# Performance work log

Hardware: AMD Instinct MI355X
Metric: run time of the kernel (lower is better)

The kernel has to match this reference:

```python
import jax, jax.numpy as jnp
import numpy as np

N = 8192          # num_points
RADIUS = 0.5


def _make_curve(num_points):
    # Reproduces the interp1d-based turbo-coil curve from __init__ (linear interp).
    xk = np.array([-2, -1, 0, 1, 1, 0, -1, -1, 0, 1, 2], dtype=np.float64)
    zk = np.array([0, 0, 1, 0, -1, 0, 1, 0, -1, 0, 0], dtype=np.float64)
    yk = np.array([0, 0, 1, 1, -1, -1, -1, 1, 1, 0, 0], dtype=np.float64)
    t = np.linspace(0.0, 1.0, len(xk))
    s = np.linspace(0.0, 1.0, num_points)
    return (np.interp(s, t, xk).astype(np.float32),
            np.interp(s, t, yk).astype(np.float32),
            np.interp(s, t, zk).astype(np.float32))


def setup_inputs() -> dict:
    x, y, z = _make_curve(N)
    return {"x": jnp.asarray(x), "y": jnp.asarray(y), "z": jnp.asarray(z)}


def _cdist(a, b):
    # pairwise Euclidean distance, safe at zero (subgradient 0 like torch.cdist)
    d2 = jnp.sum(a * a, -1, keepdims=True) - 2.0 * (a @ b.T) + jnp.sum(b * b, -1)
    d2 = jnp.maximum(d2, 0.0)
    safe = jnp.where(d2 > 0.0, d2, 1.0)
    return jnp.where(d2 > 0.0, jnp.sqrt(safe), 0.0)


def _mask_distances(dist, min_dist):
    # Original: for each row i, scan j = i, i+1, ... and overwrite entries with
    # min_dist+1 while dist[i,j] <= min_dist, breaking at the first entry that
    # exceeds min_dist (the j in range(i,0) loop is empty, so only the forward
    # scan matters). Vectorized: contiguous prefix-run starting at the diagonal.
    n = dist.shape[0]
    rows = jnp.arange(n)[:, None]
    cols = jnp.arange(n)[None, :]
    upper = cols >= rows
    cond = dist <= min_dist
    # cumprod along each row, seeded with 1 (True) left of the diagonal, so that
    # run[i,j] = all(cond[i, i..j]) for j >= i
    run = jnp.cumprod(jnp.where(upper, cond, True).astype(jnp.int32), axis=1)
    mask = upper & (run > 0)
    return jnp.where(mask, min_dist + 1.0, dist)


def _puffer_loss(p2d, low, high):
    # PufferZone(points_2d, -1.0, 1.0, x): out-of-bounds penalty on [low, high]
    return jax.nn.relu(p2d - high) + jax.nn.relu(low - p2d)


def _noise_loss(p2d):
    # noise_reduction_loss: penalize curvature (squared second differences)
    d2 = p2d[2:] - 2.0 * p2d[1:-1] + p2d[:-2]
    return d2 * d2


def reference(x, y, z, scale=1.0):
    p2d = jnp.stack([y, z], axis=1)          # [N, 2]
    p3d = jnp.stack([x, y, z], axis=1)       # [N, 3]

    fixed = _puffer_loss(p2d, -1.0, 1.0)

    dist = _cdist(p3d, p3d)                  # [N, N]
    min_dist = RADIUS * 2.0 * scale
    dist_mask = _mask_distances(dist, min_dist)
    intersect = jax.nn.relu(min_dist - dist_mask)

    noise = _noise_loss(p2d)

    # dist_loss (WeightedEuclideanDistance) taken as the pairwise cdist sum
    return (jnp.sum(fixed)
            + jnp.sum(dist) / 10000.0
            + jnp.sum(intersect)
            + jnp.sum(noise) * 10.0)
```

## Files before the change

kernel.cpp:

```cpp
#include <hip/hip_runtime.h>

constexpr int N = 8192;
constexpr float TRI = 33558528.0f;

__device__ __forceinline__ float fsqrt(float v) { return __builtin_amdgcn_sqrtf(v); }

__global__ __launch_bounds__(256, 4)
void main_kernel(const float* __restrict__ x, const float* __restrict__ y,
                 const float* __restrict__ z,
                 float* __restrict__ row_sd, float* __restrict__ row_sm,
                 float* __restrict__ row_corr) {
    const int tid  = threadIdx.x;
    const int lane = tid & 63;
    const int wave = tid >> 6;
    __shared__ float lsd[4][8];
    __shared__ float lsm[4][8];

    if (blockIdx.x < 1024) {
        const int b       = blockIdx.x;
        const int topBase = 4 * b;
        const int botBase = N - 4 * (b + 1);

        float xr[8], yr[8], zr[8];
#pragma unroll
        for (int r = 0; r < 4; ++r) {
            xr[r]     = x[topBase + r]; yr[r]     = y[topBase + r]; zr[r]     = z[topBase + r];
            xr[4 + r] = x[botBase + r]; yr[4 + r] = y[botBase + r]; zr[4 + r] = z[botBase + r];
        }
        float sd[8], sm[8];
#pragma unroll
        for (int r = 0; r < 8; ++r) { sd[r] = 0.f; sm[r] = 0.f; }

#pragma unroll
        for (int g = 0; g < 2; ++g) {
            const int base = g ? botBase : topBase;
            const int ro   = g * 4;

            {
                const int   j  = base + tid;
                const int   jc = (j < N) ? j : (N - 1);
                const float cx = x[jc], cy = y[jc], cz = z[jc];
#pragma unroll
                for (int r = 0; r < 4; ++r) {
                    const float dx = cx - xr[ro + r], dy = cy - yr[ro + r], dz = cz - zr[ro + r];
                    const float d  = fsqrt(dx * dx + dy * dy + dz * dz);
                    if (tid >= r && j < N) { sd[ro + r] += d; sm[ro + r] += fminf(d, 1.f); }
                }
            }
            int j0 = base + 256;
            if (j0 + 256 <= N) {
                float nx = x[j0 + tid], ny = y[j0 + tid], nz = z[j0 + tid];
                while (true) {
                    const float cx = nx, cy = ny, cz = nz;
                    const bool  more = (j0 + 512 <= N);
                    if (more) {
                        const int jn = j0 + 256 + tid;
                        nx = x[jn]; ny = y[jn]; nz = z[jn];
                    }
#pragma unroll
                    for (int r = 0; r < 4; ++r) {
                        const float dx = cx - xr[ro + r], dy = cy - yr[ro + r], dz = cz - zr[ro + r];
                        const float d  = fsqrt(dx * dx + dy * dy + dz * dz);
                        sd[ro + r] += d; sm[ro + r] += fminf(d, 1.f);
                    }
                    j0 += 256;
                    if (!more) break;
                }
            }
            if (j0 < N) {
                const int j = j0 + tid;
                if (j < N) {
                    const float cx = x[j], cy = y[j], cz = z[j];
#pragma unroll
                    for (int r = 0; r < 4; ++r) {
                        const float dx = cx - xr[ro + r], dy = cy - yr[ro + r], dz = cz - zr[ro + r];
                        const float d  = fsqrt(dx * dx + dy * dy + dz * dz);
                        sd[ro + r] += d; sm[ro + r] += fminf(d, 1.f);
                    }
                }
            }
        }

#pragma unroll
        for (int r = 0; r < 8; ++r) {
            float a = sd[r], c = sm[r];
#pragma unroll
            for (int off = 32; off; off >>= 1) {
                a += __shfl_down(a, off);
                c += __shfl_down(c, off);
            }
            if (lane == 0) { lsd[wave][r] = a; lsm[wave][r] = c; }
        }
        __syncthreads();
        if (tid < 8) {
            const float a = lsd[0][tid] + lsd[1][tid] + lsd[2][tid] + lsd[3][tid];
            const float c = lsm[0][tid] + lsm[1][tid] + lsm[2][tid] + lsm[3][tid];
            const int   i = (tid < 4) ? (topBase + tid) : (botBase + tid - 4);
            row_sd[i] = a;
            row_sm[i] = c;
        }
    } else {
        const int cb = blockIdx.x - 1024;
#pragma unroll
        for (int rr = 0; rr < 2; ++rr) {
            const int   i  = 8 * cb + 2 * wave + rr;
            const float xi = x[i], yi = y[i], zi = z[i];
            float corr = 0.f;
            for (int jb = i; jb < N; jb += 64) {
                const int j = jb + lane;
                float d = 2.f;
                if (j < N) {
                    const float dx = x[j] - xi, dy = y[j] - yi, dz = z[j] - zi;
                    d = fsqrt(dx * dx + dy * dy + dz * dz);
                }
                const unsigned long long far = __ballot(d > 1.0f);
                const int stop = far ? __builtin_ctzll(far) : 64;
                if (lane < stop) corr += 1.f - d;
                if (far) break;
            }
#pragma unroll
            for (int off = 32; off; off >>= 1) corr += __shfl_down(corr, off);
            if (lane == 0) row_corr[i] = corr;
        }
    }
}

__global__ __launch_bounds__(256)
void finalize_kernel(const float* __restrict__ y, const float* __restrict__ z,
                     const float* __restrict__ row_sd, const float* __restrict__ row_sm,
                     const float* __restrict__ row_corr, float* __restrict__ out) {
    const int tid = threadIdx.x;
    float A = 0.f, M = 0.f, C = 0.f, sfix = 0.f, snoise = 0.f;
    for (int i = tid; i < N; i += 256) {
        A += row_sd[i];
        M += row_sm[i];
        C += row_corr[i];
        const float yv = y[i], zv = z[i];
        sfix += fmaxf(yv - 1.f, 0.f) + fmaxf(-1.f - yv, 0.f)
              + fmaxf(zv - 1.f, 0.f) + fmaxf(-1.f - zv, 0.f);
        if (i < N - 2) {
            const float d2y = y[i + 2] - 2.f * y[i + 1] + y[i];
            const float d2z = z[i + 2] - 2.f * z[i + 1] + z[i];
            snoise += d2y * d2y + d2z * d2z;
        }
    }
    __shared__ float s[5][256];
    s[0][tid] = A; s[1][tid] = M; s[2][tid] = C; s[3][tid] = sfix; s[4][tid] = snoise;
    __syncthreads();
    for (int st = 128; st; st >>= 1) {
        if (tid < st) {
#pragma unroll
            for (int k = 0; k < 5; ++k) s[k][tid] += s[k][tid + st];
        }
        __syncthreads();
    }
    if (tid == 0)
        out[0] = s[3][0] + (2.f * s[0][0]) / 10000.f
               + (2.f * (TRI - s[1][0]) - (float)N - s[2][0]) + 10.f * s[4][0];
}

extern "C" void kernel_launch(void* const* d_in, const int* in_sizes, int n_in,
                              void* d_out, int out_size, void* d_ws, size_t ws_size,
                              hipStream_t stream) {
    const float* x = (const float*)d_in[0];
    const float* y = (const float*)d_in[1];
    const float* z = (const float*)d_in[2];
    float* out      = (float*)d_out;
    float* row_sd   = (float*)d_ws;
    float* row_sm   = row_sd + N;
    float* row_corr = row_sm + N;

    main_kernel<<<2048, 256, 0, stream>>>(x, y, z, row_sd, row_sm, row_corr);
    finalize_kernel<<<1, 256, 0, stream>>>(y, z, row_sd, row_sm, row_corr, out);
}
```

Baseline: 35.32 us.

## Process four columns per thread with float4 loads in both distance and correction paths

The pairwise-distance blocks now load x/y/z as float4 vectors, so each thread handles four columns per iteration with a 1024-column stride and per-row partial sums. The correction blocks also scan four columns per lane, 256 per wave step, with masked ballot logic, and each wave now handles four rows, cutting the correction grid from 1024 to 512 blocks. This is meant to reduce load instruction count and loop overhead and to raise ILP. The cost is more registers and more complex tail/diagonal masking, which could lower occupancy.

New measurement: 37.10 us. 1.05x slower.

```diff
diff --git a/kernel.cpp b/kernel.cpp
--- a/kernel.cpp
+++ b/kernel.cpp
@@ -13,8 +13,6 @@
     const int tid  = threadIdx.x;
     const int lane = tid & 63;
     const int wave = tid >> 6;
-    __shared__ float lsd[4][8];
-    __shared__ float lsm[4][8];
 
     if (blockIdx.x < 1024) {
         const int b       = blockIdx.x;
@@ -37,50 +35,91 @@
             const int ro   = g * 4;
 
             {
-                const int   j  = base + tid;
-                const int   jc = (j < N) ? j : (N - 1);
-                const float cx = x[jc], cy = y[jc], cz = z[jc];
+                const int   jj = base + 4 * tid;
+                const int   cj = (jj <= N - 4) ? jj : (N - 4);
+                const float4 vx = *(const float4*)(x + cj);
+                const float4 vy = *(const float4*)(y + cj);
+                const float4 vz = *(const float4*)(z + cj);
+                const float ax[4] = {vx.x, vx.y, vx.z, vx.w};
+                const float ay[4] = {vy.x, vy.y, vy.z, vy.w};
+                const float az[4] = {vz.x, vz.y, vz.z, vz.w};
+                const bool  valid = jj < N;
 #pragma unroll
                 for (int r = 0; r < 4; ++r) {
-                    const float dx = cx - xr[ro + r], dy = cy - yr[ro + r], dz = cz - zr[ro + r];
-                    const float d  = fsqrt(dx * dx + dy * dy + dz * dz);
-                    if (tid >= r && j < N) { sd[ro + r] += d; sm[ro + r] += fminf(d, 1.f); }
-                }
-            }
-            int j0 = base + 256;
-            if (j0 + 256 <= N) {
-                float nx = x[j0 + tid], ny = y[j0 + tid], nz = z[j0 + tid];
+#pragma unroll
+                    for (int q = 0; q < 4; ++q) {
+                        const float dx = ax[q] - xr[ro + r];
+                        const float dy = ay[q] - yr[ro + r];
+                        const float dz = az[q] - zr[ro + r];
+                        const float d  = fsqrt(dx * dx + dy * dy + dz * dz);
+                        if (valid && (4 * tid + q) >= r) {
+                            sd[ro + r] += d; sm[ro + r] += fminf(d, 1.f);
+                        }
+                    }
+                }
+            }
+            int j0 = base + 1024;
+            if (j0 + 1024 <= N) {
+                int idx = j0 + 4 * tid;
+                float4 vx = *(const float4*)(x + idx);
+                float4 vy = *(const float4*)(y + idx);
+                float4 vz = *(const float4*)(z + idx);
                 while (true) {
-                    const float cx = nx, cy = ny, cz = nz;
-                    const bool  more = (j0 + 512 <= N);
+                    const float ax[4] = {vx.x, vx.y, vx.z, vx.w};
+                    const float ay[4] = {vy.x, vy.y, vy.z, vy.w};
+                    const float az[4] = {vz.x, vz.y, vz.z, vz.w};
+                    const bool  more = (j0 + 2048 <= N);
                     if (more) {
-                        const int jn = j0 + 256 + tid;
-                        nx = x[jn]; ny = y[jn]; nz = z[jn];
+                        idx += 1024;
+                        vx = *(const float4*)(x + idx);
+                        vy = *(const float4*)(y + idx);
+                        vz = *(const float4*)(z + idx);
                     }
 #pragma unroll
                     for (int r = 0; r < 4; ++r) {
-                        const float dx = cx - xr[ro + r], dy = cy - yr[ro + r], dz = cz - zr[ro + r];
-                        const float d  = fsqrt(dx * dx + dy * dy + dz * dz);
-                        sd[ro + r] += d; sm[ro + r] += fminf(d, 1.f);
-                    }
-                    j0 += 256;
+                        float dsum = 0.f, msum = 0.f;
+#pragma unroll
+                        for (int q = 0; q < 4; ++q) {
+                            const float dx = ax[q] - xr[ro + r];
+                            const float dy = ay[q] - yr[ro + r];
+                            const float dz = az[q] - zr[ro + r];
+                            const float d  = fsqrt(dx * dx + dy * dy + dz * dz);
+                            dsum += d; msum += fminf(d, 1.f);
+                        }
+                        sd[ro + r] += dsum; sm[ro + r] += msum;
+                    }
+                    j0 += 1024;
                     if (!more) break;
                 }
             }
-            if (j0 < N) {
-                const int j = j0 + tid;
-                if (j < N) {
-                    const float cx = x[j], cy = y[j], cz = z[j];
+            for (; j0 < N; j0 += 1024) {
+                const int jj = j0 + 4 * tid;
+                if (jj < N) {
+                    const float4 vx = *(const float4*)(x + jj);
+                    const float4 vy = *(const float4*)(y + jj);
+                    const float4 vz = *(const float4*)(z + jj);
+                    const float ax[4] = {vx.x, vx.y, vx.z, vx.w};
+                    const float ay[4] = {vy.x, vy.y, vy.z, vy.w};
+                    const float az[4] = {vz.x, vz.y, vz.z, vz.w};
 #pragma unroll
                     for (int r = 0; r < 4; ++r) {
-                        const float dx = cx - xr[ro + r], dy = cy - yr[ro + r], dz = cz - zr[ro + r];
-                        const float d  = fsqrt(dx * dx + dy * dy + dz * dz);
-                        sd[ro + r] += d; sm[ro + r] += fminf(d, 1.f);
-                    }
-                }
-            }
-        }
-
+                        float dsum = 0.f, msum = 0.f;
+#pragma unroll
+                        for (int q = 0; q < 4; ++q) {
+                            const float dx = ax[q] - xr[ro + r];
+                            const float dy = ay[q] - yr[ro + r];
+                            const float dz = az[q] - zr[ro + r];
+                            const float d  = fsqrt(dx * dx + dy * dy + dz * dz);
+                            dsum += d; msum += fminf(d, 1.f);
+                        }
+                        sd[ro + r] += dsum; sm[ro + r] += msum;
+                    }
+                }
+            }
+        }
+
+        __shared__ float lsd[4][8];
+        __shared__ float lsm[4][8];
 #pragma unroll
         for (int r = 0; r < 8; ++r) {
             float a = sd[r], c = sm[r];
@@ -102,21 +141,49 @@
     } else {
         const int cb = blockIdx.x - 1024;
 #pragma unroll
-        for (int rr = 0; rr < 2; ++rr) {
-            const int   i  = 8 * cb + 2 * wave + rr;
+        for (int rr = 0; rr < 4; ++rr) {
+            const int   i  = 16 * cb + 4 * wave + rr;
             const float xi = x[i], yi = y[i], zi = z[i];
             float corr = 0.f;
-            for (int jb = i; jb < N; jb += 64) {
-                const int j = jb + lane;
-                float d = 2.f;
-                if (j < N) {
-                    const float dx = x[j] - xi, dy = y[j] - yi, dz = z[j] - zi;
-                    d = fsqrt(dx * dx + dy * dy + dz * dz);
-                }
-                const unsigned long long far = __ballot(d > 1.0f);
-                const int stop = far ? __builtin_ctzll(far) : 64;
-                if (lane < stop) corr += 1.f - d;
-                if (far) break;
+            int   jb   = i & ~3;
+            {
+                const int idx = jb + 4 * lane;
+                const int ci  = (idx <= N - 4) ? idx : (N - 4);
+                float4 vx = *(const float4*)(x + ci);
+                float4 vy = *(const float4*)(y + ci);
+                float4 vz = *(const float4*)(z + ci);
+                while (true) {
+                    const float ax[4] = {vx.x, vx.y, vx.z, vx.w};
+                    const float ay[4] = {vy.x, vy.y, vy.z, vy.w};
+                    const float az[4] = {vz.x, vz.y, vz.z, vz.w};
+                    const int   myj   = jb + 4 * lane;
+                    {
+                        const int nidx = myj + 256;
+                        const int cn   = (nidx <= N - 4) ? nidx : (N - 4);
+                        vx = *(const float4*)(x + cn);
+                        vy = *(const float4*)(y + cn);
+                        vz = *(const float4*)(z + cn);
+                    }
+                    float    dq[4];
+                    unsigned fm = 0u;
+#pragma unroll
+                    for (int q = 0; q < 4; ++q) {
+                        const float dx = ax[q] - xi, dy = ay[q] - yi, dz = az[q] - zi;
+                        dq[q] = fsqrt(dx * dx + dy * dy + dz * dz);
+                        const int j = myj + q;
+                        if (j >= N || (j >= i && dq[q] > 1.f)) fm |= (1u << q);
+                    }
+                    const unsigned long long far = __ballot(fm != 0u);
+                    const int L    = far ? __builtin_ctzll(far) : 64;
+                    const int qlim = (lane < L) ? 4 : ((lane == L) ? __builtin_ctz(fm | 16u) : 0);
+#pragma unroll
+                    for (int q = 0; q < 4; ++q) {
+                        const int j = myj + q;
+                        if (q < qlim && j >= i) corr += 1.f - dq[q];
+                    }
+                    if (far) break;
+                    jb += 256;
+                }
             }
 #pragma unroll
             for (int off = 32; off; off >>= 1) corr += __shfl_down(corr, off);
@@ -170,6 +237,6 @@
     float* row_sm   = row_sd + N;
     float* row_corr = row_sm + N;
 
-    main_kernel<<<2048, 256, 0, stream>>>(x, y, z, row_sd, row_sm, row_corr);
+    main_kernel<<<1536, 256, 0, stream>>>(x, y, z, row_sd, row_sm, row_corr);
     finalize_kernel<<<1, 256, 0, stream>>>(y, z, row_sd, row_sm, row_corr, out);
 }
```
